# Performance work log

Hardware: AMD Instinct MI355X
Metric: run time of the kernel (lower is better)

The kernel has to match this reference:

```python
import jax, jax.numpy as jnp
import numpy as np

B, H, L, D = 2, 16, 2048, 128

def setup_inputs() -> dict:
    key = jax.random.key(0)
    ks = jax.random.split(key, 7)
    Q = jax.random.normal(ks[0], (B, H, L, D), dtype=jnp.float32)
    K = jax.random.normal(ks[1], (B, H, L, D), dtype=jnp.float32)
    V = jax.random.normal(ks[2], (B, H, L, D), dtype=jnp.float32)
    adjacency_matrix = jax.random.uniform(ks[3], (B, L, L), dtype=jnp.float32)
    row_subtracted_distance_matrix = jax.random.uniform(ks[4], (B, L, L), dtype=jnp.float32)
    weight_A = jax.random.normal(ks[5], (1, H, 1, 1), dtype=jnp.float32)
    weight_D = jax.random.normal(ks[6], (1, H, 1, 1), dtype=jnp.float32)
    return {"Q": Q, "K": K, "V": V,
            "adjacency_matrix": adjacency_matrix,
            "row_subtracted_distance_matrix": row_subtracted_distance_matrix,
            "weight_A": weight_A, "weight_D": weight_D}

def reference(Q, K, V, adjacency_matrix, row_subtracted_distance_matrix, weight_A, weight_D):
    # Q,K,V: (b,h,l,d); A,D_s: (b,l,l) -> broadcast over heads via [:, None]
    scale = jnp.asarray(Q.shape[-1] ** 0.5, Q.dtype)
    attn_score = jnp.einsum('bhqd,bhkd->bhqk', Q, K)  # (b,h,l,l)
    A = adjacency_matrix[:, None]                      # (b,1,l,l)
    D_s = row_subtracted_distance_matrix[:, None]      # (b,1,l,l)
    # attn + attn*(A*wA) + attn*(D_s*wD) == attn * (1 + A*wA + D_s*wD)
    attn_score = attn_score * (1.0 + A * weight_A + D_s * weight_D) / scale
    attn_weight = jax.nn.softmax(attn_score, axis=-1)
    out = jnp.einsum('bhqk,bhkd->bhqd', attn_weight, V)  # dropout p=0.0 is identity
    return (out, attn_weight)
```

## Files before the change

### kernel.cpp

```cpp
#include <hip/hip_runtime.h>

constexpr int Bc = 2, Hc = 16, Lc = 2048, Dc = 128;
constexpr int BHc = Bc * Hc;
constexpr float RSCALE = 0.08838834764831845f;
constexpr size_t OUT_ELEMS = (size_t)BHc * Lc * Dc;
constexpr size_t SPLIT_ELEMS = (size_t)BHc * Lc * Dc;
constexpr size_t WS_NEED = SPLIT_ELEMS * 2 * 6;

typedef float  f32x4 __attribute__((ext_vector_type(4)));
typedef short  s16x8 __attribute__((ext_vector_type(8)));

#define AS1(p) (const __attribute__((address_space(1))) void*)(p)
#define AS3(p) (__attribute__((address_space(3))) void*)(p)

__device__ __forceinline__ ushort bf16_rne(float x) {
    unsigned u = __float_as_uint(x);
    return (ushort)((u + 0x7FFFu + ((u >> 16) & 1u)) >> 16);
}
__device__ __forceinline__ void split1(float x, ushort& h, ushort& l) {
    ushort hb = bf16_rne(x);
    float hf = __uint_as_float((unsigned)hb << 16);
    h = hb;
    l = bf16_rne(x - hf);
}

__global__ __launch_bounds__(256)
void k_split(const float* __restrict__ x, ushort* __restrict__ h, ushort* __restrict__ l)
{
    const int n4 = (int)(SPLIT_ELEMS / 4);
    const int stride = gridDim.x * blockDim.x;
    for (int i = blockIdx.x * blockDim.x + threadIdx.x; i < n4; i += stride) {
        float4 v = ((const float4*)x)[i];
        ushort4 hh, ll;
        split1(v.x, hh.x, ll.x); split1(v.y, hh.y, ll.y);
        split1(v.z, hh.z, ll.z); split1(v.w, hh.w, ll.w);
        ((ushort4*)h)[i] = hh;
        ((ushort4*)l)[i] = ll;
    }
}

__global__ __launch_bounds__(256)
void k_vsplit(const float* __restrict__ V, ushort* __restrict__ Vth, ushort* __restrict__ Vtl)
{
    __shared__ float Vs[64][132];
    const int kt = blockIdx.x, bh = blockIdx.y;
    const int k0 = kt * 64;
    const int tid = threadIdx.x;
    const float* Vb = V + ((size_t)bh * Lc + k0) * Dc;

#pragma unroll
    for (int i = 0; i < 8; i++) {
        int u = tid + 256 * i;
        int row = u >> 5, c4 = u & 31;
        float4 v = *(const float4*)(Vb + (size_t)row * Dc + c4 * 4);
        *(float4*)&Vs[row][c4 * 4] = v;
    }
    __syncthreads();

    const int d = tid >> 1, part = tid & 1;
    size_t off = ((size_t)bh * Dc + d) * Lc + k0 + part * 32;
#pragma unroll
    for (int j4 = 0; j4 < 8; j4++) {
        ushort4 hh, ll;
        split1(Vs[part * 32 + j4 * 4 + 0][d], hh.x, ll.x);
        split1(Vs[part * 32 + j4 * 4 + 1][d], hh.y, ll.y);
        split1(Vs[part * 32 + j4 * 4 + 2][d], hh.z, ll.z);
        split1(Vs[part * 32 + j4 * 4 + 3][d], hh.w, ll.w);
        *(ushort4*)(Vth + off + j4 * 4) = hh;
        *(ushort4*)(Vtl + off + j4 * 4) = ll;
    }
}

__global__ __launch_bounds__(256)
void k_scores_mfma(const ushort* __restrict__ Qh, const ushort* __restrict__ Ql,
                   const ushort* __restrict__ Kh, const ushort* __restrict__ Kl,
                   const float* __restrict__ Ag, const float* __restrict__ Dg,
                   const float* __restrict__ wAg, const float* __restrict__ wDg,
                   float* __restrict__ Sg)
{
    __shared__ ushort Qhs[128 * 32], Qls[128 * 32], Khs[128 * 32], Kls[128 * 32];

    const int kt = blockIdx.x, qt = blockIdx.y, bh = blockIdx.z;
    const int b = bh >> 4, h = bh & 15;
    const int q0 = qt * 128, k0 = kt * 128;
    const int tid = threadIdx.x;
    const int lane = tid & 63, wid = tid >> 6;
    const int wr = wid >> 1, wc = wid & 1;

    const ushort* Qhb = Qh + ((size_t)bh * Lc + q0) * Dc;
    const ushort* Qlb = Ql + ((size_t)bh * Lc + q0) * Dc;
    const ushort* Khb = Kh + ((size_t)bh * Lc + k0) * Dc;
    const ushort* Klb = Kl + ((size_t)bh * Lc + k0) * Dc;

    const int u0 = tid, u1 = tid + 256;
    const size_t g0 = (size_t)(u0 >> 2) * Dc + (u0 & 3) * 8;
    const size_t g1 = (size_t)(u1 >> 2) * Dc + (u1 & 3) * 8;
    const int l0 = u0 * 8, l1 = u1 * 8;

    f32x4 acc[4][4];
#pragma unroll
    for (int m = 0; m < 4; m++)
#pragma unroll
        for (int n = 0; n < 4; n++) acc[m][n] = (f32x4){0.f, 0.f, 0.f, 0.f};

    const int r15 = lane & 15, gkk = (lane >> 4) * 8;

    for (int c = 0; c < 4; c++) {
        const int co = c * 32;
        __builtin_amdgcn_global_load_lds(AS1(Qhb + g0 + co), AS3(&Qhs[l0]), 16, 0, 0);
        __builtin_amdgcn_global_load_lds(AS1(Qhb + g1 + co), AS3(&Qhs[l1]), 16, 0, 0);
        __builtin_amdgcn_global_load_lds(AS1(Qlb + g0 + co), AS3(&Qls[l0]), 16, 0, 0);
        __builtin_amdgcn_global_load_lds(AS1(Qlb + g1 + co), AS3(&Qls[l1]), 16, 0, 0);
        __builtin_amdgcn_global_load_lds(AS1(Khb + g0 + co), AS3(&Khs[l0]), 16, 0, 0);
        __builtin_amdgcn_global_load_lds(AS1(Khb + g1 + co), AS3(&Khs[l1]), 16, 0, 0);
        __builtin_amdgcn_global_load_lds(AS1(Klb + g0 + co), AS3(&Kls[l0]), 16, 0, 0);
        __builtin_amdgcn_global_load_lds(AS1(Klb + g1 + co), AS3(&Kls[l1]), 16, 0, 0);
        __syncthreads();

        s16x8 Ahf[4], Alf[4], Bhf[4], Blf[4];
#pragma unroll
        for (int m = 0; m < 4; m++) {
            int row = wr * 64 + m * 16 + r15;
            Ahf[m] = *(const s16x8*)&Qhs[row * 32 + gkk];
            Alf[m] = *(const s16x8*)&Qls[row * 32 + gkk];
        }
#pragma unroll
        for (int n = 0; n < 4; n++) {
            int row = wc * 64 + n * 16 + r15;
            Bhf[n] = *(const s16x8*)&Khs[row * 32 + gkk];
            Blf[n] = *(const s16x8*)&Kls[row * 32 + gkk];
        }
#pragma unroll
        for (int m = 0; m < 4; m++)
#pragma unroll
            for (int n = 0; n < 4; n++) {
                acc[m][n] = __builtin_amdgcn_mfma_f32_16x16x32_bf16(Ahf[m], Bhf[n], acc[m][n], 0, 0, 0);
                acc[m][n] = __builtin_amdgcn_mfma_f32_16x16x32_bf16(Ahf[m], Blf[n], acc[m][n], 0, 0, 0);
                acc[m][n] = __builtin_amdgcn_mfma_f32_16x16x32_bf16(Alf[m], Bhf[n], acc[m][n], 0, 0, 0);
            }
        __syncthreads();
    }

    const float wa = wAg[h], wd = wDg[h];
    const float* Arow = Ag + (size_t)b * Lc * Lc;
    const float* Drow = Dg + (size_t)b * Lc * Lc;
    float* Srow = Sg + (size_t)bh * Lc * Lc;
    const int grow = (lane >> 4) * 4;
#pragma unroll
    for (int m = 0; m < 4; m++) {
#pragma unroll
        for (int r = 0; r < 4; r++) {
            int q = q0 + wr * 64 + m * 16 + grow + r;
            size_t ro = (size_t)q * Lc + k0;
#pragma unroll
            for (int n = 0; n < 4; n++) {
                int k = wc * 64 + n * 16 + r15;
                float mult = fmaf(Arow[ro + k], wa, fmaf(Drow[ro + k], wd, 1.0f));
                Srow[ro + k] = acc[m][n][r] * mult * RSCALE;
            }
        }
    }
}

__global__ __launch_bounds__(256)
void k_softmax(float* __restrict__ Sg)
{
    __shared__ float red[8];
    const size_t row = blockIdx.x;
    float* Sr = Sg + row * (size_t)Lc;
    const int tid = threadIdx.x;
    const int w = tid >> 6;

    float4 v0 = *(const float4*)(Sr + tid * 4);
    float4 v1 = *(const float4*)(Sr + 1024 + tid * 4);

    float m = fmaxf(fmaxf(fmaxf(v0.x, v0.y), fmaxf(v0.z, v0.w)),
                    fmaxf(fmaxf(v1.x, v1.y), fmaxf(v1.z, v1.w)));
#pragma unroll
    for (int off = 32; off; off >>= 1) m = fmaxf(m, __shfl_xor(m, off));
    if ((tid & 63) == 0) red[w] = m;
    __syncthreads();
    m = fmaxf(fmaxf(red[0], red[1]), fmaxf(red[2], red[3]));

    float4 e0, e1;
    e0.x = __expf(v0.x - m); e0.y = __expf(v0.y - m);
    e0.z = __expf(v0.z - m); e0.w = __expf(v0.w - m);
    e1.x = __expf(v1.x - m); e1.y = __expf(v1.y - m);
    e1.z = __expf(v1.z - m); e1.w = __expf(v1.w - m);

    float s = e0.x + e0.y + e0.z + e0.w + e1.x + e1.y + e1.z + e1.w;
#pragma unroll
    for (int off = 32; off; off >>= 1) s += __shfl_xor(s, off);
    if ((tid & 63) == 0) red[4 + w] = s;
    __syncthreads();
    float l = red[4] + red[5] + red[6] + red[7];
    float rinv = 1.0f / l;

    e0.x *= rinv; e0.y *= rinv; e0.z *= rinv; e0.w *= rinv;
    e1.x *= rinv; e1.y *= rinv; e1.z *= rinv; e1.w *= rinv;
    *(float4*)(Sr + tid * 4) = e0;
    *(float4*)(Sr + 1024 + tid * 4) = e1;
}

__global__ __launch_bounds__(256)
void k_pv_mfma(const float* __restrict__ Pg, const ushort* __restrict__ Vth,
               const ushort* __restrict__ Vtl, float* __restrict__ Og)
{
    __shared__ ushort Phs[128 * 32], Pls[128 * 32], Vhs[128 * 32], Vls[128 * 32];

    const int qt = blockIdx.x, bh = blockIdx.y;
    const int q0 = qt * 128;
    const int tid = threadIdx.x;
    const int lane = tid & 63, wid = tid >> 6;
    const int wr = wid >> 1, wc = wid & 1;

    const float* Pb = Pg + ((size_t)bh * Lc + q0) * (size_t)Lc;
    const ushort* Vhb = Vth + (size_t)bh * Dc * Lc;
    const ushort* Vlb = Vtl + (size_t)bh * Dc * Lc;

    const int u0 = tid, u1 = tid + 256;
    const size_t vg0 = (size_t)(u0 >> 2) * Lc + (u0 & 3) * 8;
    const size_t vg1 = (size_t)(u1 >> 2) * Lc + (u1 & 3) * 8;
    const int vl0 = u0 * 8, vl1 = u1 * 8;

    f32x4 acc[4][4];
#pragma unroll
    for (int m = 0; m < 4; m++)
#pragma unroll
        for (int n = 0; n < 4; n++) acc[m][n] = (f32x4){0.f, 0.f, 0.f, 0.f};

    const int r15 = lane & 15, gkk = (lane >> 4) * 8;

    for (int k0 = 0; k0 < Lc; k0 += 32) {
        __builtin_amdgcn_global_load_lds(AS1(Vhb + vg0 + k0), AS3(&Vhs[vl0]), 16, 0, 0);
        __builtin_amdgcn_global_load_lds(AS1(Vhb + vg1 + k0), AS3(&Vhs[vl1]), 16, 0, 0);
        __builtin_amdgcn_global_load_lds(AS1(Vlb + vg0 + k0), AS3(&Vls[vl0]), 16, 0, 0);
        __builtin_amdgcn_global_load_lds(AS1(Vlb + vg1 + k0), AS3(&Vls[vl1]), 16, 0, 0);

#pragma unroll
        for (int j = 0; j < 2; j++) {
            int u = tid + 256 * j;
            int row = u >> 2, s8 = u & 3;
            const float* src = Pb + (size_t)row * Lc + k0 + s8 * 8;
            float4 a = *(const float4*)(src);
            float4 bb = *(const float4*)(src + 4);
            union { ushort us[8]; s16x8 v; } H, L;
            split1(a.x,  H.us[0], L.us[0]); split1(a.y,  H.us[1], L.us[1]);
            split1(a.z,  H.us[2], L.us[2]); split1(a.w,  H.us[3], L.us[3]);
            split1(bb.x, H.us[4], L.us[4]); split1(bb.y, H.us[5], L.us[5]);
            split1(bb.z, H.us[6], L.us[6]); split1(bb.w, H.us[7], L.us[7]);
            *(s16x8*)&Phs[row * 32 + s8 * 8] = H.v;
            *(s16x8*)&Pls[row * 32 + s8 * 8] = L.v;
        }
        __syncthreads();

        s16x8 Ah[4], Al[4], Bh[4], Bl[4];
#pragma unroll
        for (int m = 0; m < 4; m++) {
            int row = wr * 64 + m * 16 + r15;
            Ah[m] = *(const s16x8*)&Phs[row * 32 + gkk];
            Al[m] = *(const s16x8*)&Pls[row * 32 + gkk];
        }
#pragma unroll
        for (int n = 0; n < 4; n++) {
            int row = wc * 64 + n * 16 + r15;
            Bh[n] = *(const s16x8*)&Vhs[row * 32 + gkk];
            Bl[n] = *(const s16x8*)&Vls[row * 32 + gkk];
        }
#pragma unroll
        for (int m = 0; m < 4; m++)
#pragma unroll
            for (int n = 0; n < 4; n++) {
                acc[m][n] = __builtin_amdgcn_mfma_f32_16x16x32_bf16(Ah[m], Bh[n], acc[m][n], 0, 0, 0);
                acc[m][n] = __builtin_amdgcn_mfma_f32_16x16x32_bf16(Ah[m], Bl[n], acc[m][n], 0, 0, 0);
                acc[m][n] = __builtin_amdgcn_mfma_f32_16x16x32_bf16(Al[m], Bh[n], acc[m][n], 0, 0, 0);
            }
        __syncthreads();
    }

    const int grow = (lane >> 4) * 4;
#pragma unroll
    for (int m = 0; m < 4; m++) {
#pragma unroll
        for (int r = 0; r < 4; r++) {
            int q = q0 + wr * 64 + m * 16 + grow + r;
            float* Orow = Og + ((size_t)bh * Lc + q) * Dc;
#pragma unroll
            for (int n = 0; n < 4; n++)
                Orow[wc * 64 + n * 16 + r15] = acc[m][n][r];
        }
    }
}

__global__ __launch_bounds__(256)
void k_scores(const float* __restrict__ Qg, const float* __restrict__ Kg,
              const float* __restrict__ Ag, const float* __restrict__ Dg,
              const float* __restrict__ wAg, const float* __restrict__ wDg,
              float* __restrict__ Sg)
{
    __shared__ float Qs[128][36];
    __shared__ float Ks[128][36];

    const int kt = blockIdx.x, qt = blockIdx.y, bh = blockIdx.z;
    const int b = bh >> 4, h = bh & 15;
    const int q0 = qt * 128, k0 = kt * 128;
    const int tid = threadIdx.x;
    const int tx = tid & 15, ty = tid >> 4;

    const float wa = wAg[h], wd = wDg[h];
    const float* Qb = Qg + ((size_t)bh * Lc + q0) * Dc;
    const float* Kb = Kg + ((size_t)bh * Lc + k0) * Dc;

    float acc[8][8];
#pragma unroll
    for (int i = 0; i < 8; i++)
#pragma unroll
        for (int j = 0; j < 8; j++) acc[i][j] = 0.0f;

    for (int c = 0; c < 4; c++) {
#pragma unroll
        for (int i = 0; i < 4; i++) {
            int idx = tid + 256 * i;
            int row = idx >> 3;
            int c4  = idx & 7;
            float4 qv = *(const float4*)(Qb + (size_t)row * Dc + c * 32 + c4 * 4);
            float4 kv = *(const float4*)(Kb + (size_t)row * Dc + c * 32 + c4 * 4);
            *(float4*)&Qs[row][c4 * 4] = qv;
            *(float4*)&Ks[row][c4 * 4] = kv;
        }
        __syncthreads();

#pragma unroll
        for (int d4 = 0; d4 < 8; d4++) {
            float4 a[8], bbv[8];
#pragma unroll
            for (int i = 0; i < 8; i++) a[i]   = *(const float4*)&Qs[ty + 16 * i][d4 * 4];
#pragma unroll
            for (int j = 0; j < 8; j++) bbv[j] = *(const float4*)&Ks[tx + 16 * j][d4 * 4];
#pragma unroll
            for (int i = 0; i < 8; i++)
#pragma unroll
                for (int j = 0; j < 8; j++)
                    acc[i][j] += a[i].x * bbv[j].x + a[i].y * bbv[j].y
                               + a[i].z * bbv[j].z + a[i].w * bbv[j].w;
        }
        __syncthreads();
    }

    const float* Arow = Ag + (size_t)b * Lc * Lc;
    const float* Drow = Dg + (size_t)b * Lc * Lc;
    float* Srow = Sg + (size_t)bh * Lc * Lc;
#pragma unroll
    for (int i = 0; i < 8; i++) {
        int q = q0 + ty + 16 * i;
        size_t ro = (size_t)q * Lc + k0;
#pragma unroll
        for (int j = 0; j < 8; j++) {
            int k = tx + 16 * j;
            float av = Arow[ro + k];
            float dv = Drow[ro + k];
            float mult = 1.0f + av * wa + dv * wd;
            Srow[ro + k] = acc[i][j] * mult * RSCALE;
        }
    }
}

__global__ __launch_bounds__(256)
void k_pv(const float* __restrict__ Pg, const float* __restrict__ Vg,
          float* __restrict__ Og)
{
    __shared__ float Ps[128][36];
    __shared__ float Vs[32][132];

    const int qt = blockIdx.x, bh = blockIdx.y;
    const int q0 = qt * 128;
    const int tid = threadIdx.x;
    const int tx = tid & 15, ty = tid >> 4;

    const float* Pb = Pg + ((size_t)bh * Lc + q0) * (size_t)Lc;
    const float* Vb = Vg + (size_t)bh * Lc * Dc;

    float acc[8][8];
#pragma unroll
    for (int i = 0; i < 8; i++)
#pragma unroll
        for (int j = 0; j < 8; j++) acc[i][j] = 0.0f;

    for (int k0 = 0; k0 < Lc; k0 += 32) {
#pragma unroll
        for (int i = 0; i < 4; i++) {
            int idx = tid + 256 * i;
            int rowp = idx >> 3, c4p = idx & 7;
            *(float4*)&Ps[rowp][c4p * 4] =
                *(const float4*)(Pb + (size_t)rowp * Lc + k0 + c4p * 4);
            int rowv = idx >> 5, c4v = idx & 31;
            *(float4*)&Vs[rowv][c4v * 4] =
                *(const float4*)(Vb + (size_t)(k0 + rowv) * Dc + c4v * 4);
        }
        __syncthreads();

#pragma unroll
        for (int kk4 = 0; kk4 < 8; kk4++) {
            float4 a[8];
#pragma unroll
            for (int i = 0; i < 8; i++) a[i] = *(const float4*)&Ps[ty + 16 * i][kk4 * 4];
#pragma unroll
            for (int cc = 0; cc < 4; cc++) {
                int kk = kk4 * 4 + cc;
                float4 b0 = *(const float4*)&Vs[kk][tx * 4];
                float4 b1 = *(const float4*)&Vs[kk][64 + tx * 4];
#pragma unroll
                for (int i = 0; i < 8; i++) {
                    float av = (cc == 0) ? a[i].x : (cc == 1) ? a[i].y
                             : (cc == 2) ? a[i].z : a[i].w;
                    acc[i][0] += av * b0.x; acc[i][1] += av * b0.y;
                    acc[i][2] += av * b0.z; acc[i][3] += av * b0.w;
                    acc[i][4] += av * b1.x; acc[i][5] += av * b1.y;
                    acc[i][6] += av * b1.z; acc[i][7] += av * b1.w;
                }
            }
        }
        __syncthreads();
    }

#pragma unroll
    for (int i = 0; i < 8; i++) {
        int q = q0 + ty + 16 * i;
        float* Or = Og + ((size_t)bh * Lc + q) * Dc;
        *(float4*)(Or + tx * 4)      = make_float4(acc[i][0], acc[i][1], acc[i][2], acc[i][3]);
        *(float4*)(Or + 64 + tx * 4) = make_float4(acc[i][4], acc[i][5], acc[i][6], acc[i][7]);
    }
}

extern "C" void kernel_launch(void* const* d_in, const int* in_sizes, int n_in,
                              void* d_out, int out_size, void* d_ws, size_t ws_size,
                              hipStream_t stream)
{
    const float* Q  = (const float*)d_in[0];
    const float* K  = (const float*)d_in[1];
    const float* V  = (const float*)d_in[2];
    const float* A  = (const float*)d_in[3];
    const float* Ds = (const float*)d_in[4];
    const float* wA = (const float*)d_in[5];
    const float* wD = (const float*)d_in[6];

    float* out  = (float*)d_out;
    float* attn = out + OUT_ELEMS;

    if (d_ws != nullptr && ws_size >= WS_NEED) {
        ushort* Qh  = (ushort*)d_ws;
        ushort* Ql  = Qh  + SPLIT_ELEMS;
        ushort* Kh  = Ql  + SPLIT_ELEMS;
        ushort* Kl  = Kh  + SPLIT_ELEMS;
        ushort* Vth = Kl  + SPLIT_ELEMS;
        ushort* Vtl = Vth + SPLIT_ELEMS;

        hipLaunchKernelGGL(k_split, dim3(1024), dim3(256), 0, stream, Q, Qh, Ql);
        hipLaunchKernelGGL(k_split, dim3(1024), dim3(256), 0, stream, K, Kh, Kl);
        hipLaunchKernelGGL(k_vsplit, dim3(Lc / 64, BHc), dim3(256), 0, stream, V, Vth, Vtl);
        hipLaunchKernelGGL(k_scores_mfma, dim3(Lc / 128, Lc / 128, BHc), dim3(256), 0, stream,
                           Qh, Ql, Kh, Kl, A, Ds, wA, wD, attn);
        hipLaunchKernelGGL(k_softmax, dim3(BHc * Lc), dim3(256), 0, stream, attn);
        hipLaunchKernelGGL(k_pv_mfma, dim3(Lc / 128, BHc), dim3(256), 0, stream, attn, Vth, Vtl, out);
    } else {
        hipLaunchKernelGGL(k_scores, dim3(Lc / 128, Lc / 128, BHc), dim3(256), 0, stream,
                           Q, K, A, Ds, wA, wD, attn);
        hipLaunchKernelGGL(k_softmax, dim3(BHc * Lc), dim3(256), 0, stream, attn);
        hipLaunchKernelGGL(k_pv, dim3(Lc / 128, BHc), dim3(256), 0, stream, attn, V, out);
    }
}
```

Before: 1.231 ms.

## Fuse scores, softmax and PV into one kernel with in-register rows

Replaces the separate score, softmax and PV kernels with a single kernel that computes a 32-query slab's full score rows in registers. It streams double-buffered split-bf16 K tiles through LDS with swizzling, does softmax in-register, writes attention once, and accumulates PV from P staged in LDS. Q splitting moves into the kernel, dropping one launch and workspace. This removes the repeated global read/write of the large attention matrix, at the cost of heavy register and LDS use and low occupancy.

```diff
diff --git a/kernel.cpp b/kernel.cpp
--- a/kernel.cpp
+++ b/kernel.cpp
@@ -5,7 +5,7 @@
 constexpr float RSCALE = 0.08838834764831845f;
 constexpr size_t OUT_ELEMS = (size_t)BHc * Lc * Dc;
 constexpr size_t SPLIT_ELEMS = (size_t)BHc * Lc * Dc;
-constexpr size_t WS_NEED = SPLIT_ELEMS * 2 * 6;
+constexpr size_t WS_NEED = SPLIT_ELEMS * 2 * 4;
 
 typedef float  f32x4 __attribute__((ext_vector_type(4)));
 typedef short  s16x8 __attribute__((ext_vector_type(8)));
@@ -71,225 +71,251 @@
     }
 }
 
-__global__ __launch_bounds__(256)
-void k_scores_mfma(const ushort* __restrict__ Qh, const ushort* __restrict__ Ql,
-                   const ushort* __restrict__ Kh, const ushort* __restrict__ Kl,
-                   const float* __restrict__ Ag, const float* __restrict__ Dg,
-                   const float* __restrict__ wAg, const float* __restrict__ wDg,
-                   float* __restrict__ Sg)
-{
-    __shared__ ushort Qhs[128 * 32], Qls[128 * 32], Khs[128 * 32], Kls[128 * 32];
-
-    const int kt = blockIdx.x, qt = blockIdx.y, bh = blockIdx.z;
+__global__ __launch_bounds__(512, 2)
+void k_fused(const float* __restrict__ Qg,
+             const ushort* __restrict__ Kh, const ushort* __restrict__ Kl,
+             const ushort* __restrict__ Vth, const ushort* __restrict__ Vtl,
+             const float* __restrict__ Ag, const float* __restrict__ Dg,
+             const float* __restrict__ wAg, const float* __restrict__ wDg,
+             float* __restrict__ attn, float* __restrict__ Og)
+{
+    __shared__ ushort Qh_s[32 * 128], Ql_s[32 * 128];
+    __shared__ ushort Ks[2][2][128 * 128];
+    __shared__ float  red[2][8][32];
+    ushort* Ph_s = &Ks[0][0][0];
+    ushort* Pl_s = &Ks[0][1][0];
+
+    const int qt = blockIdx.x, bh = blockIdx.y;
     const int b = bh >> 4, h = bh & 15;
-    const int q0 = qt * 128, k0 = kt * 128;
+    const int q0 = qt * 32;
     const int tid = threadIdx.x;
     const int lane = tid & 63, wid = tid >> 6;
-    const int wr = wid >> 1, wc = wid & 1;
-
-    const ushort* Qhb = Qh + ((size_t)bh * Lc + q0) * Dc;
-    const ushort* Qlb = Ql + ((size_t)bh * Lc + q0) * Dc;
-    const ushort* Khb = Kh + ((size_t)bh * Lc + k0) * Dc;
-    const ushort* Klb = Kl + ((size_t)bh * Lc + k0) * Dc;
-
-    const int u0 = tid, u1 = tid + 256;
-    const size_t g0 = (size_t)(u0 >> 2) * Dc + (u0 & 3) * 8;
-    const size_t g1 = (size_t)(u1 >> 2) * Dc + (u1 & 3) * 8;
-    const int l0 = u0 * 8, l1 = u1 * 8;
-
-    f32x4 acc[4][4];
-#pragma unroll
-    for (int m = 0; m < 4; m++)
-#pragma unroll
-        for (int n = 0; n < 4; n++) acc[m][n] = (f32x4){0.f, 0.f, 0.f, 0.f};
-
-    const int r15 = lane & 15, gkk = (lane >> 4) * 8;
-
-    for (int c = 0; c < 4; c++) {
-        const int co = c * 32;
-        __builtin_amdgcn_global_load_lds(AS1(Qhb + g0 + co), AS3(&Qhs[l0]), 16, 0, 0);
-        __builtin_amdgcn_global_load_lds(AS1(Qhb + g1 + co), AS3(&Qhs[l1]), 16, 0, 0);
-        __builtin_amdgcn_global_load_lds(AS1(Qlb + g0 + co), AS3(&Qls[l0]), 16, 0, 0);
-        __builtin_amdgcn_global_load_lds(AS1(Qlb + g1 + co), AS3(&Qls[l1]), 16, 0, 0);
-        __builtin_amdgcn_global_load_lds(AS1(Khb + g0 + co), AS3(&Khs[l0]), 16, 0, 0);
-        __builtin_amdgcn_global_load_lds(AS1(Khb + g1 + co), AS3(&Khs[l1]), 16, 0, 0);
-        __builtin_amdgcn_global_load_lds(AS1(Klb + g0 + co), AS3(&Kls[l0]), 16, 0, 0);
-        __builtin_amdgcn_global_load_lds(AS1(Klb + g1 + co), AS3(&Kls[l1]), 16, 0, 0);
-        __syncthreads();
-
-        s16x8 Ahf[4], Alf[4], Bhf[4], Blf[4];
-#pragma unroll
-        for (int m = 0; m < 4; m++) {
-            int row = wr * 64 + m * 16 + r15;
-            Ahf[m] = *(const s16x8*)&Qhs[row * 32 + gkk];
-            Alf[m] = *(const s16x8*)&Qls[row * 32 + gkk];
-        }
-#pragma unroll
-        for (int n = 0; n < 4; n++) {
-            int row = wc * 64 + n * 16 + r15;
-            Bhf[n] = *(const s16x8*)&Khs[row * 32 + gkk];
-            Blf[n] = *(const s16x8*)&Kls[row * 32 + gkk];
-        }
-#pragma unroll
-        for (int m = 0; m < 4; m++)
-#pragma unroll
-            for (int n = 0; n < 4; n++) {
-                acc[m][n] = __builtin_amdgcn_mfma_f32_16x16x32_bf16(Ahf[m], Bhf[n], acc[m][n], 0, 0, 0);
-                acc[m][n] = __builtin_amdgcn_mfma_f32_16x16x32_bf16(Ahf[m], Blf[n], acc[m][n], 0, 0, 0);
-                acc[m][n] = __builtin_amdgcn_mfma_f32_16x16x32_bf16(Alf[m], Bhf[n], acc[m][n], 0, 0, 0);
+    const int l15 = lane & 15, g = lane >> 4;
+
+    const ushort* Khb = Kh + (size_t)bh * Lc * Dc;
+    const ushort* Klb = Kl + (size_t)bh * Lc * Dc;
+
+    {
+        int row = tid >> 4, s = tid & 15;
+        const float* src = Qg + ((size_t)bh * Lc + q0 + row) * Dc + s * 8;
+        float4 a = *(const float4*)src;
+        float4 c = *(const float4*)(src + 4);
+        union { ushort us[8]; s16x8 v; } H, L;
+        split1(a.x, H.us[0], L.us[0]); split1(a.y, H.us[1], L.us[1]);
+        split1(a.z, H.us[2], L.us[2]); split1(a.w, H.us[3], L.us[3]);
+        split1(c.x, H.us[4], L.us[4]); split1(c.y, H.us[5], L.us[5]);
+        split1(c.z, H.us[6], L.us[6]); split1(c.w, H.us[7], L.us[7]);
+        int p = s ^ (row & 7);
+        *(s16x8*)&Qh_s[row * 128 + p * 8] = H.v;
+        *(s16x8*)&Ql_s[row * 128 + p * 8] = L.v;
+    }
+
+#define STAGE(buf, t)                                                          \
+    {                                                                          \
+        _Pragma("unroll")                                                      \
+        for (int i = 0; i < 4; i++) {                                          \
+            int u = tid + 512 * i;                                             \
+            int row = u >> 4, p = u & 15;                                      \
+            int s = p ^ (row & 7);                                             \
+            size_t goff = (size_t)((t) * 128 + row) * Dc + s * 8;              \
+            __builtin_amdgcn_global_load_lds(AS1(Khb + goff),                  \
+                AS3(&Ks[buf][0][u * 8]), 16, 0, 0);                            \
+            __builtin_amdgcn_global_load_lds(AS1(Klb + goff),                  \
+                AS3(&Ks[buf][1][u * 8]), 16, 0, 0);                            \
+        }                                                                      \
+    }
+
+    f32x4 acc[2][16];
+#pragma unroll
+    for (int m = 0; m < 2; m++)
+#pragma unroll
+        for (int t = 0; t < 16; t++) acc[m][t] = (f32x4){0.f, 0.f, 0.f, 0.f};
+
+    STAGE(0, 0);
+    asm volatile("s_waitcnt lgkmcnt(0)" ::: "memory");
+    __builtin_amdgcn_s_barrier();
+
+    s16x8 QAh[2][4], QAl[2][4];
+#pragma unroll
+    for (int m = 0; m < 2; m++)
+#pragma unroll
+        for (int c = 0; c < 4; c++) {
+            int qrow = m * 16 + l15;
+            int sA = (c * 4 + g) ^ (qrow & 7);
+            QAh[m][c] = *(const s16x8*)&Qh_s[qrow * 128 + sA * 8];
+            QAl[m][c] = *(const s16x8*)&Ql_s[qrow * 128 + sA * 8];
+        }
+
+#pragma unroll
+    for (int t = 0; t < 16; t++) {
+        if (t < 15) STAGE((t + 1) & 1, t + 1);
+        if (t < 15) asm volatile("s_waitcnt vmcnt(8)" ::: "memory");
+        else        asm volatile("s_waitcnt vmcnt(0)" ::: "memory");
+        __builtin_amdgcn_s_barrier();
+        __builtin_amdgcn_sched_barrier(0);
+
+        const ushort* KH = &Ks[t & 1][0][0];
+        const ushort* KL = &Ks[t & 1][1][0];
+        const int krow = wid * 16 + l15;
+        __builtin_amdgcn_s_setprio(1);
+#pragma unroll
+        for (int c = 0; c < 4; c++) {
+            int sB = (c * 4 + g) ^ (krow & 7);
+            s16x8 Bh = *(const s16x8*)&KH[krow * 128 + sB * 8];
+            s16x8 Bl = *(const s16x8*)&KL[krow * 128 + sB * 8];
+#pragma unroll
+            for (int m = 0; m < 2; m++) {
+                acc[m][t] = __builtin_amdgcn_mfma_f32_16x16x32_bf16(QAh[m][c], Bh, acc[m][t], 0, 0, 0);
+                acc[m][t] = __builtin_amdgcn_mfma_f32_16x16x32_bf16(QAh[m][c], Bl, acc[m][t], 0, 0, 0);
+                acc[m][t] = __builtin_amdgcn_mfma_f32_16x16x32_bf16(QAl[m][c], Bh, acc[m][t], 0, 0, 0);
+            }
+        }
+        __builtin_amdgcn_s_setprio(0);
+        __builtin_amdgcn_sched_barrier(0);
+        __builtin_amdgcn_s_barrier();
+    }
+
+    const float wa = wAg[h], wd = wDg[h];
+    const float* Ab = Ag + (size_t)b * Lc * Lc;
+    const float* Db = Dg + (size_t)b * Lc * Lc;
+#pragma unroll
+    for (int t = 0; t < 16; t++) {
+        int col = t * 128 + wid * 16 + l15;
+#pragma unroll
+        for (int m = 0; m < 2; m++)
+#pragma unroll
+            for (int r = 0; r < 4; r++) {
+                int q = q0 + m * 16 + g * 4 + r;
+                size_t off = (size_t)q * Lc + col;
+                float mult = fmaf(Ab[off], wa, fmaf(Db[off], wd, 1.0f));
+                acc[m][t][r] *= mult * RSCALE;
+            }
+    }
+
+    float mrow[2][4];
+#pragma unroll
+    for (int m = 0; m < 2; m++)
+#pragma unroll
+        for (int r = 0; r < 4; r++) {
+            float mv = acc[m][0][r];
+#pragma unroll
+            for (int t = 1; t < 16; t++) mv = fmaxf(mv, acc[m][t][r]);
+#pragma unroll
+            for (int mask = 1; mask < 16; mask <<= 1) mv = fmaxf(mv, __shfl_xor(mv, mask));
+            mrow[m][r] = mv;
+        }
+    if (l15 == 0) {
+#pragma unroll
+        for (int m = 0; m < 2; m++)
+#pragma unroll
+            for (int r = 0; r < 4; r++) red[0][wid][m * 16 + g * 4 + r] = mrow[m][r];
+    }
+    __syncthreads();
+#pragma unroll
+    for (int m = 0; m < 2; m++)
+#pragma unroll
+        for (int r = 0; r < 4; r++) {
+            int row = m * 16 + g * 4 + r;
+            float mm = red[0][0][row];
+#pragma unroll
+            for (int w = 1; w < 8; w++) mm = fmaxf(mm, red[0][w][row]);
+            mrow[m][r] = mm;
+        }
+
+    float lrow[2][4];
+#pragma unroll
+    for (int m = 0; m < 2; m++)
+#pragma unroll
+        for (int r = 0; r < 4; r++) {
+            float sv = 0.f;
+#pragma unroll
+            for (int t = 0; t < 16; t++) {
+                float e = __expf(acc[m][t][r] - mrow[m][r]);
+                acc[m][t][r] = e;
+                sv += e;
+            }
+#pragma unroll
+            for (int mask = 1; mask < 16; mask <<= 1) sv += __shfl_xor(sv, mask);
+            lrow[m][r] = sv;
+        }
+    if (l15 == 0) {
+#pragma unroll
+        for (int m = 0; m < 2; m++)
+#pragma unroll
+            for (int r = 0; r < 4; r++) red[1][wid][m * 16 + g * 4 + r] = lrow[m][r];
+    }
+    __syncthreads();
+#pragma unroll
+    for (int m = 0; m < 2; m++)
+#pragma unroll
+        for (int r = 0; r < 4; r++) {
+            int row = m * 16 + g * 4 + r;
+            float ss = red[1][0][row];
+#pragma unroll
+            for (int w = 1; w < 8; w++) ss += red[1][w][row];
+            float rinv = 1.0f / ss;
+#pragma unroll
+            for (int t = 0; t < 16; t++) acc[m][t][r] *= rinv;
+        }
+
+    const ushort* Vhb = Vth + (size_t)bh * Dc * Lc;
+    const ushort* Vlb = Vtl + (size_t)bh * Dc * Lc;
+    float* attnb = attn + ((size_t)bh * Lc + q0) * Lc;
+
+    f32x4 oacc[2];
+    oacc[0] = (f32x4){0.f, 0.f, 0.f, 0.f};
+    oacc[1] = (f32x4){0.f, 0.f, 0.f, 0.f};
+
+    __syncthreads();
+
+#pragma unroll
+    for (int t = 0; t < 16; t++) {
+        const int kk = wid * 16 + l15;
+#pragma unroll
+        for (int m = 0; m < 2; m++)
+#pragma unroll
+            for (int r = 0; r < 4; r++) {
+                int q = m * 16 + g * 4 + r;
+                float p = acc[m][t][r];
+                attnb[(size_t)q * Lc + t * 128 + kk] = p;
+                ushort hu, lu;
+                split1(p, hu, lu);
+                int seg = (kk >> 3) ^ (q & 7);
+                Ph_s[q * 128 + seg * 8 + (kk & 7)] = hu;
+                Pl_s[q * 128 + seg * 8 + (kk & 7)] = lu;
             }
         __syncthreads();
-    }
-
-    const float wa = wAg[h], wd = wDg[h];
-    const float* Arow = Ag + (size_t)b * Lc * Lc;
-    const float* Drow = Dg + (size_t)b * Lc * Lc;
-    float* Srow = Sg + (size_t)bh * Lc * Lc;
-    const int grow = (lane >> 4) * 4;
-#pragma unroll
-    for (int m = 0; m < 4; m++) {
+
+        __builtin_amdgcn_s_setprio(1);
+#pragma unroll
+        for (int kc = 0; kc < 4; kc++) {
+            const int dd = wid * 16 + l15;
+            size_t voff = (size_t)dd * Lc + t * 128 + kc * 32 + g * 8;
+            s16x8 Bh = *(const s16x8*)(Vhb + voff);
+            s16x8 Bl = *(const s16x8*)(Vlb + voff);
+#pragma unroll
+            for (int m = 0; m < 2; m++) {
+                int qrow = m * 16 + l15;
+                int sP = (kc * 4 + g) ^ (qrow & 7);
+                s16x8 Ph = *(const s16x8*)&Ph_s[qrow * 128 + sP * 8];
+                s16x8 Pl = *(const s16x8*)&Pl_s[qrow * 128 + sP * 8];
+                oacc[m] = __builtin_amdgcn_mfma_f32_16x16x32_bf16(Ph, Bh, oacc[m], 0, 0, 0);
+                oacc[m] = __builtin_amdgcn_mfma_f32_16x16x32_bf16(Ph, Bl, oacc[m], 0, 0, 0);
+                oacc[m] = __builtin_amdgcn_mfma_f32_16x16x32_bf16(Pl, Bh, oacc[m], 0, 0, 0);
+            }
+        }
+        __builtin_amdgcn_s_setprio(0);
+        __syncthreads();
+    }
+
+#pragma unroll
+    for (int m = 0; m < 2; m++)
 #pragma unroll
         for (int r = 0; r < 4; r++) {
-            int q = q0 + wr * 64 + m * 16 + grow + r;
-            size_t ro = (size_t)q * Lc + k0;
-#pragma unroll
-            for (int n = 0; n < 4; n++) {
-                int k = wc * 64 + n * 16 + r15;
-                float mult = fmaf(Arow[ro + k], wa, fmaf(Drow[ro + k], wd, 1.0f));
-                Srow[ro + k] = acc[m][n][r] * mult * RSCALE;
-            }
-        }
-    }
-}
-
-__global__ __launch_bounds__(256)
-void k_softmax(float* __restrict__ Sg)
-{
-    __shared__ float red[8];
-    const size_t row = blockIdx.x;
-    float* Sr = Sg + row * (size_t)Lc;
-    const int tid = threadIdx.x;
-    const int w = tid >> 6;
-
-    float4 v0 = *(const float4*)(Sr + tid * 4);
-    float4 v1 = *(const float4*)(Sr + 1024 + tid * 4);
-
-    float m = fmaxf(fmaxf(fmaxf(v0.x, v0.y), fmaxf(v0.z, v0.w)),
-                    fmaxf(fmaxf(v1.x, v1.y), fmaxf(v1.z, v1.w)));
-#pragma unroll
-    for (int off = 32; off; off >>= 1) m = fmaxf(m, __shfl_xor(m, off));
-    if ((tid & 63) == 0) red[w] = m;
-    __syncthreads();
-    m = fmaxf(fmaxf(red[0], red[1]), fmaxf(red[2], red[3]));
-
-    float4 e0, e1;
-    e0.x = __expf(v0.x - m); e0.y = __expf(v0.y - m);
-    e0.z = __expf(v0.z - m); e0.w = __expf(v0.w - m);
-    e1.x = __expf(v1.x - m); e1.y = __expf(v1.y - m);
-    e1.z = __expf(v1.z - m); e1.w = __expf(v1.w - m);
-
-    float s = e0.x + e0.y + e0.z + e0.w + e1.x + e1.y + e1.z + e1.w;
-#pragma unroll
-    for (int off = 32; off; off >>= 1) s += __shfl_xor(s, off);
-    if ((tid & 63) == 0) red[4 + w] = s;
-    __syncthreads();
-    float l = red[4] + red[5] + red[6] + red[7];
-    float rinv = 1.0f / l;
-
-    e0.x *= rinv; e0.y *= rinv; e0.z *= rinv; e0.w *= rinv;
-    e1.x *= rinv; e1.y *= rinv; e1.z *= rinv; e1.w *= rinv;
-    *(float4*)(Sr + tid * 4) = e0;
-    *(float4*)(Sr + 1024 + tid * 4) = e1;
-}
-
-__global__ __launch_bounds__(256)
-void k_pv_mfma(const float* __restrict__ Pg, const ushort* __restrict__ Vth,
-               const ushort* __restrict__ Vtl, float* __restrict__ Og)
-{
-    __shared__ ushort Phs[128 * 32], Pls[128 * 32], Vhs[128 * 32], Vls[128 * 32];
-
-    const int qt = blockIdx.x, bh = blockIdx.y;
-    const int q0 = qt * 128;
-    const int tid = threadIdx.x;
-    const int lane = tid & 63, wid = tid >> 6;
-    const int wr = wid >> 1, wc = wid & 1;
-
-    const float* Pb = Pg + ((size_t)bh * Lc + q0) * (size_t)Lc;
-    const ushort* Vhb = Vth + (size_t)bh * Dc * Lc;
-    const ushort* Vlb = Vtl + (size_t)bh * Dc * Lc;
-
-    const int u0 = tid, u1 = tid + 256;
-    const size_t vg0 = (size_t)(u0 >> 2) * Lc + (u0 & 3) * 8;
-    const size_t vg1 = (size_t)(u1 >> 2) * Lc + (u1 & 3) * 8;
-    const int vl0 = u0 * 8, vl1 = u1 * 8;
-
-    f32x4 acc[4][4];
-#pragma unroll
-    for (int m = 0; m < 4; m++)
-#pragma unroll
-        for (int n = 0; n < 4; n++) acc[m][n] = (f32x4){0.f, 0.f, 0.f, 0.f};
-
-    const int r15 = lane & 15, gkk = (lane >> 4) * 8;
-
-    for (int k0 = 0; k0 < Lc; k0 += 32) {
-        __builtin_amdgcn_global_load_lds(AS1(Vhb + vg0 + k0), AS3(&Vhs[vl0]), 16, 0, 0);
-        __builtin_amdgcn_global_load_lds(AS1(Vhb + vg1 + k0), AS3(&Vhs[vl1]), 16, 0, 0);
-        __builtin_amdgcn_global_load_lds(AS1(Vlb + vg0 + k0), AS3(&Vls[vl0]), 16, 0, 0);
-        __builtin_amdgcn_global_load_lds(AS1(Vlb + vg1 + k0), AS3(&Vls[vl1]), 16, 0, 0);
-
-#pragma unroll
-        for (int j = 0; j < 2; j++) {
-            int u = tid + 256 * j;
-            int row = u >> 2, s8 = u & 3;
-            const float* src = Pb + (size_t)row * Lc + k0 + s8 * 8;
-            float4 a = *(const float4*)(src);
-            float4 bb = *(const float4*)(src + 4);
-            union { ushort us[8]; s16x8 v; } H, L;
-            split1(a.x,  H.us[0], L.us[0]); split1(a.y,  H.us[1], L.us[1]);
-            split1(a.z,  H.us[2], L.us[2]); split1(a.w,  H.us[3], L.us[3]);
-            split1(bb.x, H.us[4], L.us[4]); split1(bb.y, H.us[5], L.us[5]);
-            split1(bb.z, H.us[6], L.us[6]); split1(bb.w, H.us[7], L.us[7]);
-            *(s16x8*)&Phs[row * 32 + s8 * 8] = H.v;
-            *(s16x8*)&Pls[row * 32 + s8 * 8] = L.v;
-        }
-        __syncthreads();
-
-        s16x8 Ah[4], Al[4], Bh[4], Bl[4];
-#pragma unroll
-        for (int m = 0; m < 4; m++) {
-            int row = wr * 64 + m * 16 + r15;
-            Ah[m] = *(const s16x8*)&Phs[row * 32 + gkk];
-            Al[m] = *(const s16x8*)&Pls[row * 32 + gkk];
-        }
-#pragma unroll
-        for (int n = 0; n < 4; n++) {
-            int row = wc * 64 + n * 16 + r15;
-            Bh[n] = *(const s16x8*)&Vhs[row * 32 + gkk];
-            Bl[n] = *(const s16x8*)&Vls[row * 32 + gkk];
-        }
-#pragma unroll
-        for (int m = 0; m < 4; m++)
-#pragma unroll
-            for (int n = 0; n < 4; n++) {
-                acc[m][n] = __builtin_amdgcn_mfma_f32_16x16x32_bf16(Ah[m], Bh[n], acc[m][n], 0, 0, 0);
-                acc[m][n] = __builtin_amdgcn_mfma_f32_16x16x32_bf16(Ah[m], Bl[n], acc[m][n], 0, 0, 0);
-                acc[m][n] = __builtin_amdgcn_mfma_f32_16x16x32_bf16(Al[m], Bh[n], acc[m][n], 0, 0, 0);
-            }
-        __syncthreads();
-    }
-
-    const int grow = (lane >> 4) * 4;
-#pragma unroll
-    for (int m = 0; m < 4; m++) {
-#pragma unroll
-        for (int r = 0; r < 4; r++) {
-            int q = q0 + wr * 64 + m * 16 + grow + r;
-            float* Orow = Og + ((size_t)bh * Lc + q) * Dc;
-#pragma unroll
-            for (int n = 0; n < 4; n++)
-                Orow[wc * 64 + n * 16 + r15] = acc[m][n][r];
-        }
-    }
+            int q = q0 + m * 16 + g * 4 + r;
+            Og[((size_t)bh * Lc + q) * Dc + wid * 16 + l15] = oacc[m][r];
+        }
+#undef STAGE
 }
 
 __global__ __launch_bounds__(256)
@@ -299,7 +325,7 @@
               float* __restrict__ Sg)
 {
     __shared__ float Qs[128][36];
-    __shared__ float Ks[128][36];
+    __shared__ float Ks2[128][36];
 
     const int kt = blockIdx.x, qt = blockIdx.y, bh = blockIdx.z;
     const int b = bh >> 4, h = bh & 15;
@@ -326,7 +352,7 @@
             float4 qv = *(const float4*)(Qb + (size_t)row * Dc + c * 32 + c4 * 4);
             float4 kv = *(const float4*)(Kb + (size_t)row * Dc + c * 32 + c4 * 4);
             *(float4*)&Qs[row][c4 * 4] = qv;
-            *(float4*)&Ks[row][c4 * 4] = kv;
+            *(float4*)&Ks2[row][c4 * 4] = kv;
         }
         __syncthreads();
 
@@ -336,7 +362,7 @@
 #pragma unroll
             for (int i = 0; i < 8; i++) a[i]   = *(const float4*)&Qs[ty + 16 * i][d4 * 4];
 #pragma unroll
-            for (int j = 0; j < 8; j++) bbv[j] = *(const float4*)&Ks[tx + 16 * j][d4 * 4];
+            for (int j = 0; j < 8; j++) bbv[j] = *(const float4*)&Ks2[tx + 16 * j][d4 * 4];
 #pragma unroll
             for (int i = 0; i < 8; i++)
 #pragma unroll
@@ -363,6 +389,46 @@
             Srow[ro + k] = acc[i][j] * mult * RSCALE;
         }
     }
+}
+
+__global__ __launch_bounds__(256)
+void k_softmax(float* __restrict__ Sg)
+{
+    __shared__ float red[8];
+    const size_t row = blockIdx.x;
+    float* Sr = Sg + row * (size_t)Lc;
+    const int tid = threadIdx.x;
+    const int w = tid >> 6;
+
+    float4 v0 = *(const float4*)(Sr + tid * 4);
+    float4 v1 = *(const float4*)(Sr + 1024 + tid * 4);
+
+    float m = fmaxf(fmaxf(fmaxf(v0.x, v0.y), fmaxf(v0.z, v0.w)),
+                    fmaxf(fmaxf(v1.x, v1.y), fmaxf(v1.z, v1.w)));
+#pragma unroll
+    for (int off = 32; off; off >>= 1) m = fmaxf(m, __shfl_xor(m, off));
+    if ((tid & 63) == 0) red[w] = m;
+    __syncthreads();
+    m = fmaxf(fmaxf(red[0], red[1]), fmaxf(red[2], red[3]));
+
+    float4 e0, e1;
+    e0.x = __expf(v0.x - m); e0.y = __expf(v0.y - m);
+    e0.z = __expf(v0.z - m); e0.w = __expf(v0.w - m);
+    e1.x = __expf(v1.x - m); e1.y = __expf(v1.y - m);
+    e1.z = __expf(v1.z - m); e1.w = __expf(v1.w - m);
+
+    float s = e0.x + e0.y + e0.z + e0.w + e1.x + e1.y + e1.z + e1.w;
+#pragma unroll
+    for (int off = 32; off; off >>= 1) s += __shfl_xor(s, off);
+    if ((tid & 63) == 0) red[4 + w] = s;
+    __syncthreads();
+    float l = red[4] + red[5] + red[6] + red[7];
+    float rinv = 1.0f / l;
+
+    e0.x *= rinv; e0.y *= rinv; e0.z *= rinv; e0.w *= rinv;
+    e1.x *= rinv; e1.y *= rinv; e1.z *= rinv; e1.w *= rinv;
+    *(float4*)(Sr + tid * 4) = e0;
+    *(float4*)(Sr + 1024 + tid * 4) = e1;
 }
 
 __global__ __launch_bounds__(256)
@@ -448,20 +514,15 @@
     float* attn = out + OUT_ELEMS;
 
     if (d_ws != nullptr && ws_size >= WS_NEED) {
-        ushort* Qh  = (ushort*)d_ws;
-        ushort* Ql  = Qh  + SPLIT_ELEMS;
-        ushort* Kh  = Ql  + SPLIT_ELEMS;
+        ushort* Kh  = (ushort*)d_ws;
         ushort* Kl  = Kh  + SPLIT_ELEMS;
         ushort* Vth = Kl  + SPLIT_ELEMS;
         ushort* Vtl = Vth + SPLIT_ELEMS;
 
-        hipLaunchKernelGGL(k_split, dim3(1024), dim3(256), 0, stream, Q, Qh, Ql);
         hipLaunchKernelGGL(k_split, dim3(1024), dim3(256), 0, stream, K, Kh, Kl);
         hipLaunchKernelGGL(k_vsplit, dim3(Lc / 64, BHc), dim3(256), 0, stream, V, Vth, Vtl);
-        hipLaunchKernelGGL(k_scores_mfma, dim3(Lc / 128, Lc / 128, BHc), dim3(256), 0, stream,
-                           Qh, Ql, Kh, Kl, A, Ds, wA, wD, attn);
-        hipLaunchKernelGGL(k_softmax, dim3(BHc * Lc), dim3(256), 0, stream, attn);
-        hipLaunchKernelGGL(k_pv_mfma, dim3(Lc / 128, BHc), dim3(256), 0, stream, attn, Vth, Vtl, out);
+        hipLaunchKernelGGL(k_fused, dim3(Lc / 32, BHc), dim3(512), 0, stream,
+                           Q, Kh, Kl, Vth, Vtl, A, Ds, wA, wD, attn, out);
     } else {
         hipLaunchKernelGGL(k_scores, dim3(Lc / 128, Lc / 128, BHc), dim3(256), 0, stream,
                            Q, K, A, Ds, wA, wD, attn);
```

After: 1.317 ms. +7.0%, slower.
